# Kernel tuning notes

Measured on AMD Instinct MI355X. Metric: run time of the kernel, lower is better.

Reference implementation:

```python
import jax, jax.numpy as jnp
import numpy as np

N, E, IN, OUT, EF = 20000, 100000, 32, 32, 16
NEG = -1e30  # finite sentinel for masked scores (avoids inf*0 grads)


def setup_inputs() -> dict:
    key = jax.random.key(0)
    ks = jax.random.split(key, 8)
    return {
        "feat": jax.random.normal(ks[0], (N, IN), jnp.float32),
        "efeat": jax.random.normal(ks[1], (E, EF), jnp.float32),
        "src": jax.random.randint(ks[2], (E,), 0, N, dtype=jnp.int32),
        "dst": jax.random.randint(ks[3], (E,), 0, N, dtype=jnp.int32),
        "etype": jax.random.randint(ks[4], (E,), 0, 2, dtype=jnp.int32),
        "attn_w": jax.random.normal(ks[5], (2 * IN, 1), jnp.float32) * 0.1,
        "attn_b": jnp.zeros((1,), jnp.float32),
        "ef1_w": jax.random.normal(ks[6], (EF, IN * OUT), jnp.float32) * 0.05,
        "ef1_b": jnp.zeros((IN * OUT,), jnp.float32),
        "ef2_w": jax.random.normal(ks[7], (EF, IN * OUT), jnp.float32) * 0.05,
        "ef2_b": jnp.zeros((IN * OUT,), jnp.float32),
        "bias": jnp.zeros((OUT,), jnp.float32),
    }


def reference(feat, efeat, src, dst, etype, attn_w, attn_b,
              ef1_w, ef1_b, ef2_w, ef2_b, bias):
    n_nodes = feat.shape[0]
    z_src = feat[src]                      # [E, IN] gather src features
    z_dst = feat[dst]                      # [E, IN] gather dst features
    # per-edge scalar attention score: leaky_relu(Linear(cat(z_src, z_dst)))
    score = jax.nn.leaky_relu(
        (jnp.concatenate([z_src, z_dst], axis=1) @ attn_w + attn_b)[:, 0]
    )  # [E]

    def relation_agg(mask, w, b):
        # edge-specific weight matrices: [E, IN, OUT]
        We = (efeat @ w + b).reshape(E, IN, OUT)
        # message per edge = src_feat @ W_e  (sum over IN commutes with attn)
        msg = jnp.einsum('ei,eio->eo', z_src, We)        # [E, OUT]
        # segment softmax over incoming edges of this relation per dst node
        s = jnp.where(mask, score, NEG)
        smax = jax.ops.segment_max(s, dst, num_segments=n_nodes)
        ex = jnp.where(mask, jnp.exp(s - smax[dst]), 0.0)
        den = jax.ops.segment_sum(ex, dst, num_segments=n_nodes)
        alpha = ex / jnp.where(den > 0, den, 1.0)[dst]   # [E]
        # attention-weighted scatter-sum to dst nodes
        return jax.ops.segment_sum(alpha[:, None] * msg, dst,
                                   num_segments=n_nodes)  # [N, OUT]

    rst = relation_agg(etype == 0, ef1_w, ef1_b) \
        + relation_agg(etype == 1, ef2_w, ef2_b) \
        + bias
    return rst
```

## Files before the change

### kernel.cpp

```cpp
#include <hip/hip_runtime.h>

typedef __attribute__((ext_vector_type(8))) short bf16x8;
typedef __attribute__((ext_vector_type(16))) float f32x16;

__device__ __forceinline__ unsigned short f2b(float x) {
    unsigned u = __float_as_uint(x);
    unsigned r = (u + 0x7fffu + ((u >> 16) & 1u)) >> 16;
    return (unsigned short)r;
}
__device__ __forceinline__ unsigned f2b2(float lo, float hi) {
    return (unsigned)f2b(lo) | ((unsigned)f2b(hi) << 16);
}
__device__ __forceinline__ float b2f(unsigned short u) {
    return __uint_as_float((unsigned)u << 16);
}

__global__ void k_zero(int* __restrict__ hist,
                       const float* __restrict__ feat, const float* __restrict__ attn_w,
                       const float* __restrict__ w1, const float* __restrict__ b1,
                       const float* __restrict__ w2, const float* __restrict__ b2,
                       float* __restrict__ ps, float* __restrict__ pd,
                       unsigned short* __restrict__ PA, int N) {
    int idx = blockIdx.x * blockDim.x + threadIdx.x;
    int n2q = (2 * N + 3) >> 2;
    if (idx < n2q) ((int4*)hist)[idx] = make_int4(0, 0, 0, 0);
    if (idx < N) {
        const float4* zp = (const float4*)(feat + (long)idx * 32);
        const float4* aw = (const float4*)attn_w;
        float a = 0.f, b = 0.f;
        #pragma unroll
        for (int j = 0; j < 8; ++j) {
            float4 z = zp[j], wa = aw[j], wb = aw[8 + j];
            a = fmaf(z.x, wa.x, a); a = fmaf(z.y, wa.y, a);
            a = fmaf(z.z, wa.z, a); a = fmaf(z.w, wa.w, a);
            b = fmaf(z.x, wb.x, b); b = fmaf(z.y, wb.y, b);
            b = fmaf(z.z, wb.z, b); b = fmaf(z.w, wb.w, b);
        }
        ps[idx] = a; pd[idx] = b;
    }
    if (idx < 2 * 17 * 2 * 64) {
        int l = idx & 63;
        int x = idx >> 6;
        int h = x & 1; x >>= 1;
        int t = x % 17;
        int r = x / 17;
        const float* W = r ? w2 : w1;
        const float* B = r ? b2 : b1;
        int o = l & 31;
        int kb = h * 16 + (l >> 5) * 8;
        unsigned short v[8];
        #pragma unroll
        for (int j = 0; j < 8; ++j) {
            int i = kb + j;
            float sv = (t < 16) ? W[t * 1024 + i * 32 + o] : B[i * 32 + o];
            v[j] = f2b(sv);
        }
        uint4 pack;
        pack.x = (unsigned)v[0] | ((unsigned)v[1] << 16);
        pack.y = (unsigned)v[2] | ((unsigned)v[3] << 16);
        pack.z = (unsigned)v[4] | ((unsigned)v[5] << 16);
        pack.w = (unsigned)v[6] | ((unsigned)v[7] << 16);
        *((uint4*)PA + idx) = pack;
    }
}

__global__ void k_hist(const int* __restrict__ dst, const int* __restrict__ etype,
                       int* __restrict__ hist, int E, int N) {
    int e = blockIdx.x * blockDim.x + threadIdx.x;
    if (e < E) atomicAdd(&hist[etype[e] * N + dst[e]], 1);
}

__global__ __launch_bounds__(256) void k_scan1(const int* __restrict__ hist,
                                               int* __restrict__ rowptr,
                                               int* __restrict__ bsum, int n) {
    __shared__ int s[256];
    int t = threadIdx.x;
    int i0 = blockIdx.x * 1024 + t * 4;
    int4 hv = make_int4(0, 0, 0, 0);
    if (i0 + 3 < n) hv = *(const int4*)(hist + i0);
    else {
        if (i0 + 0 < n) hv.x = hist[i0 + 0];
        if (i0 + 1 < n) hv.y = hist[i0 + 1];
        if (i0 + 2 < n) hv.z = hist[i0 + 2];
        if (i0 + 3 < n) hv.w = hist[i0 + 3];
    }
    int tot = hv.x + hv.y + hv.z + hv.w;
    s[t] = tot;
    __syncthreads();
    for (int d = 1; d < 256; d <<= 1) {
        int x = (t >= d) ? s[t - d] : 0;
        __syncthreads();
        s[t] += x;
        __syncthreads();
    }
    int run = s[t] - tot;
    if (i0 + 0 < n) rowptr[i0 + 0] = run; run += hv.x;
    if (i0 + 1 < n) rowptr[i0 + 1] = run; run += hv.y;
    if (i0 + 2 < n) rowptr[i0 + 2] = run; run += hv.z;
    if (i0 + 3 < n) rowptr[i0 + 3] = run;
    if (t == 255) bsum[blockIdx.x] = s[255];
}

__global__ void k_scanB(int* __restrict__ rowptr, const int* __restrict__ bsum,
                        int* __restrict__ cursor, int n, int E, int nb) {
    __shared__ int soff;
    int i = blockIdx.x * blockDim.x + threadIdx.x;
    if (threadIdx.x < 64) {
        int g = (blockIdx.x * 256) >> 10;
        int v = (threadIdx.x < min(g, nb)) ? bsum[threadIdx.x] : 0;
        #pragma unroll
        for (int d = 32; d >= 1; d >>= 1) v += __shfl_down(v, d);
        if (threadIdx.x == 0) soff = v;
    }
    __syncthreads();
    int off = soff;
    if (i < n) {
        int v = rowptr[i] + off;
        rowptr[i] = v;
        cursor[i] = v;
    }
    if (i == 0) rowptr[n] = E;
}

__global__ void k_score(const int* __restrict__ src, const int* __restrict__ dst,
                        const int* __restrict__ etype,
                        const float* __restrict__ ps, const float* __restrict__ pd,
                        const float* __restrict__ attn_b,
                        int* __restrict__ cursor, int* __restrict__ sortidx,
                        float* __restrict__ exs, int E, int N) {
    int e = blockIdx.x * blockDim.x + threadIdx.x;
    if (e >= E) return;
    int d = dst[e];
    float sc = ps[src[e]] + pd[d] + attn_b[0];
    sc = sc >= 0.f ? sc : 0.01f * sc;
    float v = __expf(sc);
    int key = etype[e] * N + d;
    int pos = atomicAdd(&cursor[key], 1);
    sortidx[pos] = e;
    exs[pos] = v;
}

__global__ __launch_bounds__(256) void k_msg(
    const float* __restrict__ feat, const float* __restrict__ efeat,
    const int* __restrict__ src, const unsigned short* __restrict__ PA,
    const int* __restrict__ sortidx, const int* __restrict__ rowptr,
    unsigned short* __restrict__ wmsg, int E, int N) {
    int r = blockIdx.y;
    int cnt0 = rowptr[N];
    int relstart = r ? cnt0 : 0;
    int count = r ? (E - cnt0) : cnt0;
    int base = blockIdx.x * 128;
    if (count <= 0 || base >= count) return;

    __shared__ __align__(16) char smem[18432];
    unsigned short (*z_bf)[32] = (unsigned short(*)[32])smem;
    float (*ut)[128] = (float(*)[128])(smem + 8192);
    float (*msgl)[36] = (float(*)[36])smem;

    int tid = threadIdx.x;
    {
        int el = tid >> 1, half = tid & 1;
        int gi = base + el;
        int e = sortidx[relstart + min(gi, count - 1)];
        int sn = src[e];
        const float4* zp = (const float4*)(feat + (long)sn * 32 + half * 16);
        float4 a0 = zp[0], a1 = zp[1], a2 = zp[2], a3 = zp[3];
        uint4 p0, p1;
        p0.x = f2b2(a0.x, a0.y); p0.y = f2b2(a0.z, a0.w);
        p0.z = f2b2(a1.x, a1.y); p0.w = f2b2(a1.z, a1.w);
        p1.x = f2b2(a2.x, a2.y); p1.y = f2b2(a2.z, a2.w);
        p1.z = f2b2(a3.x, a3.y); p1.w = f2b2(a3.z, a3.w);
        uint4* zd = (uint4*)&z_bf[el][half * 16];
        zd[0] = p0; zd[1] = p1;
        const float4* up = (const float4*)(efeat + (long)e * 16 + half * 8);
        float4 c0 = up[0], c1 = up[1];
        int fb = half * 8;
        ut[fb + 0][el] = c0.x; ut[fb + 1][el] = c0.y;
        ut[fb + 2][el] = c0.z; ut[fb + 3][el] = c0.w;
        ut[fb + 4][el] = c1.x; ut[fb + 5][el] = c1.y;
        ut[fb + 6][el] = c1.z; ut[fb + 7][el] = c1.w;
    }
    __syncthreads();

    int lane = tid & 63;
    int ecol = (tid >> 6) * 32 + (lane & 31);
    int kb = (lane >> 5) * 8;
    bf16x8 b0 = *(const bf16x8*)&z_bf[ecol][kb];
    bf16x8 b1 = *(const bf16x8*)&z_bf[ecol][16 + kb];

    const bf16x8* pa = (const bf16x8*)PA + (long)r * 34 * 64 + lane;

    f32x16 msg;
    {
        bf16x8 a0 = pa[32 * 64];
        bf16x8 a1 = pa[33 * 64];
        f32x16 c;
        #pragma unroll
        for (int k = 0; k < 16; ++k) c[k] = 0.f;
        c = __builtin_amdgcn_mfma_f32_32x32x16_bf16(a0, b0, c, 0, 0, 0);
        c = __builtin_amdgcn_mfma_f32_32x32x16_bf16(a1, b1, c, 0, 0, 0);
        msg = c;
    }
    float uu[16];
    #pragma unroll
    for (int t = 0; t < 16; ++t) uu[t] = ut[t][ecol];
    #pragma unroll 4
    for (int t = 0; t < 16; ++t) {
        bf16x8 a0 = pa[(t * 2 + 0) * 64];
        bf16x8 a1 = pa[(t * 2 + 1) * 64];
        f32x16 c;
        #pragma unroll
        for (int k = 0; k < 16; ++k) c[k] = 0.f;
        c = __builtin_amdgcn_mfma_f32_32x32x16_bf16(a0, b0, c, 0, 0, 0);
        c = __builtin_amdgcn_mfma_f32_32x32x16_bf16(a1, b1, c, 0, 0, 0);
        #pragma unroll
        for (int k = 0; k < 16; ++k) msg[k] = fmaf(uu[t], c[k], msg[k]);
    }
    __syncthreads();

    {
        int ob = 4 * (lane >> 5);
        float4* mq = (float4*)&msgl[ecol][ob];
        mq[0] = make_float4(msg[0],  msg[1],  msg[2],  msg[3]);
        mq[2] = make_float4(msg[4],  msg[5],  msg[6],  msg[7]);
        mq[4] = make_float4(msg[8],  msg[9],  msg[10], msg[11]);
        mq[6] = make_float4(msg[12], msg[13], msg[14], msg[15]);
    }
    __syncthreads();

    {
        uint4* wb = (uint4*)(wmsg + (long)(relstart + base) * 32);
        #pragma unroll
        for (int j = 0; j < 2; ++j) {
            int flat = j * 256 + tid;
            int row = flat >> 2, col = (flat & 3) * 8;
            if (base + row < count) {
                const float* mr = &msgl[row][col];
                uint4 pk;
                pk.x = f2b2(mr[0], mr[1]);
                pk.y = f2b2(mr[2], mr[3]);
                pk.z = f2b2(mr[4], mr[5]);
                pk.w = f2b2(mr[6], mr[7]);
                wb[flat] = pk;
            }
        }
    }
}

__global__ void k_reduce(const int* __restrict__ rowptr, const float* __restrict__ exs,
                         const unsigned short* __restrict__ wmsg,
                         const float* __restrict__ bias,
                         float* __restrict__ out, int N) {
    int tid = blockIdx.x * blockDim.x + threadIdx.x;
    if (tid >= N * 8) return;
    int n = tid >> 3, og = tid & 7;
    float4 acc = ((const float4*)bias)[og];
    #pragma unroll 1
    for (int r = 0; r < 2; ++r) {
        int k = r * N + n;
        int s = rowptr[k], e2 = rowptr[k + 1];
        if (s >= e2) continue;
        float den = 0.f;
        #pragma unroll 1
        for (int p = s; p < e2; ++p) den += exs[p];
        float inv = 1.f / den;
        #pragma unroll 1
        for (int p = s; p < e2; ++p) {
            float w = exs[p] * inv;
            ushort4 m = *(const ushort4*)(wmsg + (long)p * 32 + og * 4);
            acc.x = fmaf(w, b2f(m.x), acc.x);
            acc.y = fmaf(w, b2f(m.y), acc.y);
            acc.z = fmaf(w, b2f(m.z), acc.z);
            acc.w = fmaf(w, b2f(m.w), acc.w);
        }
    }
    ((float4*)out)[tid] = acc;
}

extern "C" void kernel_launch(void* const* d_in, const int* in_sizes, int n_in,
                              void* d_out, int out_size, void* d_ws, size_t ws_size,
                              hipStream_t stream) {
    const float* feat   = (const float*)d_in[0];
    const float* efeat  = (const float*)d_in[1];
    const int*   src    = (const int*)d_in[2];
    const int*   dst    = (const int*)d_in[3];
    const int*   etype  = (const int*)d_in[4];
    const float* attn_w = (const float*)d_in[5];
    const float* attn_b = (const float*)d_in[6];
    const float* ef1_w  = (const float*)d_in[7];
    const float* ef1_b  = (const float*)d_in[8];
    const float* ef2_w  = (const float*)d_in[9];
    const float* ef2_b  = (const float*)d_in[10];
    const float* bias   = (const float*)d_in[11];

    int E = in_sizes[2];
    int N = in_sizes[0] / 32;
    int n2 = 2 * N;
    int nb = (n2 + 1023) / 1024;

    float*          ps      = (float*)d_ws;
    float*          pd      = ps + N;
    unsigned short* PA      = (unsigned short*)(pd + N);
    int*            hist    = (int*)(PA + 2 * 17 * 2 * 64 * 8);
    int*            rowptr  = hist + n2;
    int*            cursor  = rowptr + n2 + 1;
    int*            bsum    = cursor + n2;
    int*            sortidx = bsum + 64;
    float*          exs     = (float*)(sortidx + E);
    unsigned short* wmsg    = (unsigned short*)(((size_t)(exs + E) + 15) & ~(size_t)15);
    float*          out     = (float*)d_out;

    k_zero<<<(N + 255) / 256, 256, 0, stream>>>(hist, feat, attn_w,
                                                ef1_w, ef1_b, ef2_w, ef2_b,
                                                ps, pd, PA, N);
    k_hist<<<(E + 255) / 256, 256, 0, stream>>>(dst, etype, hist, E, N);
    k_scan1<<<nb, 256, 0, stream>>>(hist, rowptr, bsum, n2);
    k_scanB<<<(n2 + 255) / 256, 256, 0, stream>>>(rowptr, bsum, cursor, n2, E, nb);
    k_score<<<(E + 255) / 256, 256, 0, stream>>>(src, dst, etype, ps, pd, attn_b,
                                                 cursor, sortidx, exs, E, N);
    dim3 mgrid((E + 127) / 128, 2);
    k_msg<<<mgrid, 256, 0, stream>>>(feat, efeat, src, PA, sortidx, rowptr,
                                     wmsg, E, N);
    k_reduce<<<(N * 8 + 255) / 256, 256, 0, stream>>>(rowptr, exs, wmsg, bias, out, N);
}
```

Measured before the change: 48.89 us.

## Fuse scan into single-pass decoupled lookback, atomically accumulate softmax denominators, use packed FMA

The two-kernel scan becomes one kernel. Each block publishes its total through a lookback flag array and spins on earlier blocks' flags to get its offset, which removes one launch. The softmax denominator is now built with float atomics in the score kernel, so the reduce kernel no longer makes a separate pass over exs. The message accumulation in k_msg uses v_pk_fma_f32 on float pairs. The risks are added atomic contention on den, spin-waiting that relies on all earlier blocks being scheduled, and a non-deterministic float summation order.

```diff
diff --git a/kernel.cpp b/kernel.cpp
--- a/kernel.cpp
+++ b/kernel.cpp
@@ -2,6 +2,7 @@
 
 typedef __attribute__((ext_vector_type(8))) short bf16x8;
 typedef __attribute__((ext_vector_type(16))) float f32x16;
+typedef __attribute__((ext_vector_type(2))) float f32x2;
 
 __device__ __forceinline__ unsigned short f2b(float x) {
     unsigned u = __float_as_uint(x);
@@ -14,16 +15,22 @@
 __device__ __forceinline__ float b2f(unsigned short u) {
     return __uint_as_float((unsigned)u << 16);
 }
-
-__global__ void k_zero(int* __restrict__ hist,
+__device__ __forceinline__ f32x2 pk_fma(f32x2 a, f32x2 b, f32x2 c) {
+    f32x2 d;
+    asm("v_pk_fma_f32 %0, %1, %2, %3" : "=v"(d) : "v"(a), "v"(b), "v"(c));
+    return d;
+}
+
+__global__ void k_zero(int* __restrict__ histden, int* __restrict__ lkb,
                        const float* __restrict__ feat, const float* __restrict__ attn_w,
                        const float* __restrict__ w1, const float* __restrict__ b1,
                        const float* __restrict__ w2, const float* __restrict__ b2,
                        float* __restrict__ ps, float* __restrict__ pd,
                        unsigned short* __restrict__ PA, int N) {
     int idx = blockIdx.x * blockDim.x + threadIdx.x;
-    int n2q = (2 * N + 3) >> 2;
-    if (idx < n2q) ((int4*)hist)[idx] = make_int4(0, 0, 0, 0);
+    int n4q = N;
+    if (idx < n4q) ((int4*)histden)[idx] = make_int4(0, 0, 0, 0);
+    if (idx < 16) ((int4*)lkb)[idx] = make_int4(0, 0, 0, 0);
     if (idx < N) {
         const float4* zp = (const float4*)(feat + (long)idx * 32);
         const float4* aw = (const float4*)attn_w;
@@ -70,12 +77,14 @@
     if (e < E) atomicAdd(&hist[etype[e] * N + dst[e]], 1);
 }
 
-__global__ __launch_bounds__(256) void k_scan1(const int* __restrict__ hist,
-                                               int* __restrict__ rowptr,
-                                               int* __restrict__ bsum, int n) {
+__global__ __launch_bounds__(256) void k_scan(const int* __restrict__ hist,
+                                              int* __restrict__ rowptr,
+                                              int* __restrict__ cursor,
+                                              int* __restrict__ lkb, int n, int E) {
     __shared__ int s[256];
-    int t = threadIdx.x;
-    int i0 = blockIdx.x * 1024 + t * 4;
+    __shared__ int soff;
+    int t = threadIdx.x, b = blockIdx.x;
+    int i0 = b * 1024 + t * 4;
     int4 hv = make_int4(0, 0, 0, 0);
     if (i0 + 3 < n) hv = *(const int4*)(hist + i0);
     else {
@@ -93,41 +102,34 @@
         s[t] += x;
         __syncthreads();
     }
-    int run = s[t] - tot;
-    if (i0 + 0 < n) rowptr[i0 + 0] = run; run += hv.x;
-    if (i0 + 1 < n) rowptr[i0 + 1] = run; run += hv.y;
-    if (i0 + 2 < n) rowptr[i0 + 2] = run; run += hv.z;
-    if (i0 + 3 < n) rowptr[i0 + 3] = run;
-    if (t == 255) bsum[blockIdx.x] = s[255];
-}
-
-__global__ void k_scanB(int* __restrict__ rowptr, const int* __restrict__ bsum,
-                        int* __restrict__ cursor, int n, int E, int nb) {
-    __shared__ int soff;
-    int i = blockIdx.x * blockDim.x + threadIdx.x;
-    if (threadIdx.x < 64) {
-        int g = (blockIdx.x * 256) >> 10;
-        int v = (threadIdx.x < min(g, nb)) ? bsum[threadIdx.x] : 0;
+    if (t == 255) atomicExch(&lkb[b], s[255] + 1);
+    if (t < 64) {
+        int v = 0;
+        if (t < b) {
+            int p;
+            do { p = atomicAdd(&lkb[t], 0); } while (p == 0);
+            v = p - 1;
+        }
         #pragma unroll
         for (int d = 32; d >= 1; d >>= 1) v += __shfl_down(v, d);
-        if (threadIdx.x == 0) soff = v;
-    }
-    __syncthreads();
-    int off = soff;
-    if (i < n) {
-        int v = rowptr[i] + off;
-        rowptr[i] = v;
-        cursor[i] = v;
-    }
-    if (i == 0) rowptr[n] = E;
+        if (t == 0) soff = v;
+    }
+    __syncthreads();
+    int run = s[t] - tot + soff;
+    if (i0 + 0 < n) { rowptr[i0 + 0] = run; cursor[i0 + 0] = run; } run += hv.x;
+    if (i0 + 1 < n) { rowptr[i0 + 1] = run; cursor[i0 + 1] = run; } run += hv.y;
+    if (i0 + 2 < n) { rowptr[i0 + 2] = run; cursor[i0 + 2] = run; } run += hv.z;
+    if (i0 + 3 < n) { rowptr[i0 + 3] = run; cursor[i0 + 3] = run; }
+    if (t == 0 && b == 0) rowptr[n] = E;
 }
 
 __global__ void k_score(const int* __restrict__ src, const int* __restrict__ dst,
                         const int* __restrict__ etype,
                         const float* __restrict__ ps, const float* __restrict__ pd,
                         const float* __restrict__ attn_b,
-                        int* __restrict__ cursor, int* __restrict__ sortidx,
-                        float* __restrict__ exs, int E, int N) {
+                        int* __restrict__ cursor, float* __restrict__ den,
+                        int* __restrict__ sortidx, float* __restrict__ exs,
+                        int E, int N) {
     int e = blockIdx.x * blockDim.x + threadIdx.x;
     if (e >= E) return;
     int d = dst[e];
@@ -135,6 +137,7 @@
     sc = sc >= 0.f ? sc : 0.01f * sc;
     float v = __expf(sc);
     int key = etype[e] * N + d;
+    atomicAdd(&den[key], v);
     int pos = atomicAdd(&cursor[key], 1);
     sortidx[pos] = e;
     exs[pos] = v;
@@ -188,9 +191,13 @@
     bf16x8 b0 = *(const bf16x8*)&z_bf[ecol][kb];
     bf16x8 b1 = *(const bf16x8*)&z_bf[ecol][16 + kb];
 
+    float uu[16];
+    #pragma unroll
+    for (int t = 0; t < 16; ++t) uu[t] = ut[t][ecol];
+
     const bf16x8* pa = (const bf16x8*)PA + (long)r * 34 * 64 + lane;
 
-    f32x16 msg;
+    f32x2 m2[8];
     {
         bf16x8 a0 = pa[32 * 64];
         bf16x8 a1 = pa[33 * 64];
@@ -199,11 +206,9 @@
         for (int k = 0; k < 16; ++k) c[k] = 0.f;
         c = __builtin_amdgcn_mfma_f32_32x32x16_bf16(a0, b0, c, 0, 0, 0);
         c = __builtin_amdgcn_mfma_f32_32x32x16_bf16(a1, b1, c, 0, 0, 0);
-        msg = c;
-    }
-    float uu[16];
-    #pragma unroll
-    for (int t = 0; t < 16; ++t) uu[t] = ut[t][ecol];
+        #pragma unroll
+        for (int k = 0; k < 8; ++k) { m2[k][0] = c[2 * k]; m2[k][1] = c[2 * k + 1]; }
+    }
     #pragma unroll 4
     for (int t = 0; t < 16; ++t) {
         bf16x8 a0 = pa[(t * 2 + 0) * 64];
@@ -213,18 +218,22 @@
         for (int k = 0; k < 16; ++k) c[k] = 0.f;
         c = __builtin_amdgcn_mfma_f32_32x32x16_bf16(a0, b0, c, 0, 0, 0);
         c = __builtin_amdgcn_mfma_f32_32x32x16_bf16(a1, b1, c, 0, 0, 0);
-        #pragma unroll
-        for (int k = 0; k < 16; ++k) msg[k] = fmaf(uu[t], c[k], msg[k]);
+        f32x2 ud; ud[0] = uu[t]; ud[1] = uu[t];
+        #pragma unroll
+        for (int k = 0; k < 8; ++k) {
+            f32x2 cc; cc[0] = c[2 * k]; cc[1] = c[2 * k + 1];
+            m2[k] = pk_fma(ud, cc, m2[k]);
+        }
     }
     __syncthreads();
 
     {
         int ob = 4 * (lane >> 5);
         float4* mq = (float4*)&msgl[ecol][ob];
-        mq[0] = make_float4(msg[0],  msg[1],  msg[2],  msg[3]);
-        mq[2] = make_float4(msg[4],  msg[5],  msg[6],  msg[7]);
-        mq[4] = make_float4(msg[8],  msg[9],  msg[10], msg[11]);
-        mq[6] = make_float4(msg[12], msg[13], msg[14], msg[15]);
+        mq[0] = make_float4(m2[0][0], m2[0][1], m2[1][0], m2[1][1]);
+        mq[2] = make_float4(m2[2][0], m2[2][1], m2[3][0], m2[3][1]);
+        mq[4] = make_float4(m2[4][0], m2[4][1], m2[5][0], m2[5][1]);
+        mq[6] = make_float4(m2[6][0], m2[6][1], m2[7][0], m2[7][1]);
     }
     __syncthreads();
 
@@ -248,6 +257,7 @@
 }
 
 __global__ void k_reduce(const int* __restrict__ rowptr, const float* __restrict__ exs,
+                         const float* __restrict__ den,
                          const unsigned short* __restrict__ wmsg,
                          const float* __restrict__ bias,
                          float* __restrict__ out, int N) {
@@ -260,10 +270,7 @@
         int k = r * N + n;
         int s = rowptr[k], e2 = rowptr[k + 1];
         if (s >= e2) continue;
-        float den = 0.f;
-        #pragma unroll 1
-        for (int p = s; p < e2; ++p) den += exs[p];
-        float inv = 1.f / den;
+        float inv = 1.f / den[k];
         #pragma unroll 1
         for (int p = s; p < e2; ++p) {
             float w = exs[p] * inv;
@@ -302,24 +309,24 @@
     float*          pd      = ps + N;
     unsigned short* PA      = (unsigned short*)(pd + N);
     int*            hist    = (int*)(PA + 2 * 17 * 2 * 64 * 8);
-    int*            rowptr  = hist + n2;
+    float*          den     = (float*)(hist + n2);
+    int*            rowptr  = (int*)(den + n2);
     int*            cursor  = rowptr + n2 + 1;
-    int*            bsum    = cursor + n2;
-    int*            sortidx = bsum + 64;
+    int*            lkb     = cursor + n2;
+    int*            sortidx = lkb + 64;
     float*          exs     = (float*)(sortidx + E);
     unsigned short* wmsg    = (unsigned short*)(((size_t)(exs + E) + 15) & ~(size_t)15);
     float*          out     = (float*)d_out;
 
-    k_zero<<<(N + 255) / 256, 256, 0, stream>>>(hist, feat, attn_w,
+    k_zero<<<(N + 255) / 256, 256, 0, stream>>>(hist, lkb, feat, attn_w,
                                                 ef1_w, ef1_b, ef2_w, ef2_b,
                                                 ps, pd, PA, N);
     k_hist<<<(E + 255) / 256, 256, 0, stream>>>(dst, etype, hist, E, N);
-    k_scan1<<<nb, 256, 0, stream>>>(hist, rowptr, bsum, n2);
-    k_scanB<<<(n2 + 255) / 256, 256, 0, stream>>>(rowptr, bsum, cursor, n2, E, nb);
+    k_scan<<<nb, 256, 0, stream>>>(hist, rowptr, cursor, lkb, n2, E);
     k_score<<<(E + 255) / 256, 256, 0, stream>>>(src, dst, etype, ps, pd, attn_b,
-                                                 cursor, sortidx, exs, E, N);
+                                                 cursor, den, sortidx, exs, E, N);
     dim3 mgrid((E + 127) / 128, 2);
     k_msg<<<mgrid, 256, 0, stream>>>(feat, efeat, src, PA, sortidx, rowptr,
                                      wmsg, E, N);
-    k_reduce<<<(N * 8 + 255) / 256, 256, 0, stream>>>(rowptr, exs, wmsg, bias, out, N);
-}
+    k_reduce<<<(N * 8 + 255) / 256, 256, 0, stream>>>(rowptr, exs, den, wmsg, bias, out, N);
+}
```

Measured after the change: 52.98 us. +8.4%, slower.
